# Performance work log

Measured on AMD Instinct MI355X. Metric: run time of the kernel, lower is better.

Reference implementation:

```python
import jax, jax.numpy as jnp
import numpy as np

B, V, HP, WP = 1, 6, 37, 66
N, CD, CC = HP * WP, 768, 256
BEVH = BEVW = 100
Q = BEVH * BEVW
NH, NP, D, Z = 8, 4, 4, 8
HD = CC // NH
PC = (-51.2, -51.2, -5.0, 51.2, 51.2, 3.0)
SCALE, PT, PL = 0.5775, 0.0, 0.0
H2, W2 = 518, 924
EPS = 1e-6


def setup_inputs() -> dict:
    key = jax.random.key(0)
    ks = jax.random.split(key, 10)
    s = 0.02
    return {
        "last_tokens": jax.random.normal(ks[0], (B, V, N, CD), jnp.float32),
        "lidar2img": jax.random.normal(ks[1], (B, V, 4, 4), jnp.float32),
        "proj_w": jax.random.normal(ks[2], (CC, CD), jnp.float32) * s,
        "bev_query": jax.random.normal(ks[3], (Q, CC), jnp.float32) * s,
        "w_view": jnp.zeros((1, V, 1), jnp.float32),
        "vp_w": jax.random.normal(ks[4], (CC, CC), jnp.float32) * s,
        "vp_b": jnp.zeros((CC,), jnp.float32),
        "so_w": jax.random.normal(ks[5], (NH * NP * 2, CC), jnp.float32) * s,
        "so_b": jnp.zeros((NH * NP * 2,), jnp.float32),
        "aw_w": jax.random.normal(ks[6], (NH * NP, CC), jnp.float32) * s,
        "aw_b": jnp.zeros((NH * NP,), jnp.float32),
        "op_w": jax.random.normal(ks[7], (CC, CC), jnp.float32) * s,
        "op_b": jnp.zeros((CC,), jnp.float32),
    }


def _ref_points_3d():
    # normalized pillar reference points, (D, Q, 3) in xyz order, Q = h*BEVW + w
    xs = (jnp.arange(BEVW, dtype=jnp.float32) + 0.5) / BEVW
    ys = (jnp.arange(BEVH, dtype=jnp.float32) + 0.5) / BEVH
    zs = jnp.linspace(0.5, Z - 0.5, D, dtype=jnp.float32) / Z
    gx = jnp.broadcast_to(xs[None, :], (BEVH, BEVW)).reshape(-1)
    gy = jnp.broadcast_to(ys[:, None], (BEVH, BEVW)).reshape(-1)
    return jnp.stack([jnp.broadcast_to(gx, (D, Q)),
                      jnp.broadcast_to(gy, (D, Q)),
                      jnp.broadcast_to(zs[:, None], (D, Q))], axis=-1)


def reference(last_tokens, lidar2img, proj_w, bev_query, w_view,
              vp_w, vp_b, so_w, so_b, aw_w, aw_b, op_w, op_b):
    BV = B * V
    # ---- project 3D BEV pillar points to camera views ----
    ref = _ref_points_3d()  # (D, Q, 3)
    wx = ref[..., 0] * (PC[3] - PC[0]) + PC[0]
    wy = ref[..., 1] * (PC[4] - PC[1]) + PC[1]
    wz = ref[..., 2] * (PC[5] - PC[2]) + PC[2]
    ref4 = jnp.stack([wx, wy, wz, jnp.ones_like(wx)], axis=-1)  # (D, Q, 4)
    cam = jnp.einsum('bvij,dqj->bvdqi', lidar2img, ref4)  # (B, V, D, Q, 4)
    depth = cam[..., 2]
    bev_mask = depth > 1e-5
    uv = cam[..., :2] / jnp.clip(depth, 1e-5)[..., None]
    u = uv[..., 0] * SCALE + PL
    v = uv[..., 1] * SCALE + PT
    in_img = (u >= 0) & (u <= W2 - 1) & (v >= 0) & (v <= H2 - 1)
    valid = bev_mask & in_img
    refx = jnp.clip(u / max(W2 - 1.0, 1.0), 0.0, 1.0)
    refy = jnp.clip(v / max(H2 - 1.0, 1.0), 0.0, 1.0)
    w = jnp.maximum(valid.astype(jnp.float32), EPS)  # (B, V, D, Q)
    den = jnp.maximum(w.sum(2), EPS)
    rx = (refx * w).sum(2) / den
    ry = (refy * w).sum(2) / den
    ref2d = jnp.stack([rx, ry], axis=-1).reshape(BV, Q, 2)

    # ---- value features: 1x1 conv proj + value_proj ----
    val = jnp.einsum('bvnc,oc->bvno', last_tokens, proj_w).reshape(BV, N, CC)
    val = val @ vp_w.T + vp_b
    val = val.reshape(BV, N, NH, HD)

    # ---- deformable attention (single level) ----
    query = jnp.broadcast_to(bev_query[None], (BV, Q, CC))
    off = (query @ so_w.T + so_b).reshape(BV, Q, NH, NP, 2)
    attn = jax.nn.softmax((query @ aw_w.T + aw_b).reshape(BV, Q, NH, NP), axis=-1)
    normalizer = jnp.array([WP, HP], jnp.float32)
    loc = ref2d[:, :, None, None, :] + off / normalizer  # (BV, Q, NH, NP, 2)

    # bilinear sampling, grid_sample semantics (align_corners=False, zero pad)
    x = loc[..., 0] * WP - 0.5
    y = loc[..., 1] * HP - 0.5
    x0 = jnp.floor(x); y0 = jnp.floor(y)
    fx = x - x0; fy = y - y0
    x0i = x0.astype(jnp.int32); y0i = y0.astype(jnp.int32)
    b_idx = jnp.arange(BV)[:, None, None, None]
    h_idx = jnp.arange(NH)[None, None, :, None]

    def corner(xi, yi, wgt):
        ok = ((xi >= 0) & (xi < WP) & (yi >= 0) & (yi < HP)).astype(val.dtype)
        lin = jnp.clip(yi, 0, HP - 1) * WP + jnp.clip(xi, 0, WP - 1)
        g = val[b_idx, lin, h_idx]  # (BV, Q, NH, NP, HD)
        return g * (ok * wgt)[..., None]

    samp = (corner(x0i, y0i, (1 - fx) * (1 - fy))
            + corner(x0i + 1, y0i, fx * (1 - fy))
            + corner(x0i, y0i + 1, (1 - fx) * fy)
            + corner(x0i + 1, y0i + 1, fx * fy))
    out = (samp * attn[..., None]).sum(3).reshape(BV, Q, CC)
    out = out @ op_w.T + op_b + query  # residual (mmcv identity)

    # ---- view-weighted combine ----
    out = out.reshape(B, V, Q, CC)
    wv = jax.nn.softplus(w_view)  # (1, V, 1)
    num = (out * wv[..., None]).sum(1)  # (B, Q, CC)
    den_v = jnp.maximum(wv.sum(1), EPS)[..., None]
    bev = num / den_v
    return jnp.transpose(bev, (0, 2, 1)).reshape(B, CC, BEVH, BEVW)
```

## Files before the change

### kernel.cpp

```cpp
#include <hip/hip_runtime.h>
#include <math.h>

#define Q_TOT 10000
#define NVIEW 6
#define NTOK  2442
#define HP_   37
#define WP_   66
#define CD_   768
#define CC_   256

typedef __attribute__((ext_vector_type(8))) short bf16x8;
typedef __attribute__((ext_vector_type(4))) float f32x4;

__device__ inline unsigned f2bf(float f) {
    unsigned u = __builtin_bit_cast(unsigned, f);
    unsigned r = u + 0x7FFFu + ((u >> 16) & 1u);
    return r >> 16;
}

__global__ __launch_bounds__(256) void w2_kernel(const float* __restrict__ vp_w,
                                                 const float* __restrict__ proj_w,
                                                 unsigned short* __restrict__ W2b) {
    int b = blockIdx.x;
    int o2 = b / 3;
    int c = (b % 3) * 256 + threadIdx.x;
    __shared__ float vps[256];
    vps[threadIdx.x] = vp_w[(size_t)o2 * 256 + threadIdx.x];
    __syncthreads();
    float acc = 0.f;
#pragma unroll 16
    for (int o = 0; o < 256; ++o) {
        acc += vps[o] * proj_w[(size_t)o * CD_ + c];
    }
    W2b[(size_t)o2 * CD_ + c] = (unsigned short)f2bf(acc);
}

__global__ void cvt8_kernel(const float* __restrict__ src, unsigned short* __restrict__ dst, int n8) {
    int i = blockIdx.x * blockDim.x + threadIdx.x;
    if (i >= n8) return;
    float4 a = *(const float4*)(src + (size_t)i * 8);
    float4 b = *(const float4*)(src + (size_t)i * 8 + 4);
    uint4 o;
    o.x = f2bf(a.x) | (f2bf(a.y) << 16);
    o.y = f2bf(a.z) | (f2bf(a.w) << 16);
    o.z = f2bf(b.x) | (f2bf(b.y) << 16);
    o.w = f2bf(b.z) | (f2bf(b.w) << 16);
    *(uint4*)(dst + (size_t)i * 8) = o;
}

__global__ void ref2d_kernel(const float* __restrict__ l2i, float* __restrict__ ref2d) {
    int idx = blockIdx.x * blockDim.x + threadIdx.x;
    if (idx >= NVIEW * Q_TOT) return;
    int v = idx / Q_TOT, q = idx % Q_TOT;
    int wq = q % 100, hq = q / 100;
    float gx = (wq + 0.5f) * 0.01f;
    float gy = (hq + 0.5f) * 0.01f;
    float wx = gx * 102.4f - 51.2f;
    float wy = gy * 102.4f - 51.2f;
    const float* L = l2i + v * 16;
    float L0=L[0],L1=L[1],L2=L[2],L3=L[3],L4=L[4],L5=L[5],L6=L[6],L7=L[7];
    float L8=L[8],L9=L[9],L10=L[10],L11=L[11];
    float sw = 0.f, sx = 0.f, sy = 0.f;
#pragma unroll
    for (int d = 0; d < 4; ++d) {
        float zs = (0.5f + (float)d * (7.0f / 3.0f)) * 0.125f;
        float wz = zs * 8.0f - 5.0f;
        float c0 = L0 * wx + L1 * wy + L2 * wz + L3;
        float c1 = L4 * wx + L5 * wy + L6 * wz + L7;
        float c2 = L8 * wx + L9 * wy + L10 * wz + L11;
        bool bm = c2 > 1e-5f;
        float dc = fmaxf(c2, 1e-5f);
        float u  = (c0 / dc) * 0.5775f;
        float vv = (c1 / dc) * 0.5775f;
        bool in_img = (u >= 0.f) && (u <= 923.f) && (vv >= 0.f) && (vv <= 517.f);
        bool valid = bm && in_img;
        float refx = fminf(fmaxf(u / 923.0f, 0.f), 1.f);
        float refy = fminf(fmaxf(vv / 517.0f, 0.f), 1.f);
        float w = valid ? 1.0f : 1e-6f;
        sw += w; sx += refx * w; sy += refy * w;
    }
    float den = fmaxf(sw, 1e-6f);
    ref2d[(size_t)idx * 2 + 0] = sx / den;
    ref2d[(size_t)idx * 2 + 1] = sy / den;
}

__global__ void concatb_kernel(const float* __restrict__ so_w, const float* __restrict__ so_b,
                               const float* __restrict__ aw_w, const float* __restrict__ aw_b,
                               const float* __restrict__ wview,
                               unsigned short* __restrict__ WQb, float* __restrict__ bqp,
                               float* __restrict__ vwn) {
    int row = blockIdx.x, col = threadIdx.x;
    float v = (row < 64) ? so_w[row * 256 + col] : (row < 96 ? aw_w[(row - 64) * 256 + col] : 0.f);
    WQb[row * 256 + col] = (unsigned short)f2bf(v);
    if (row == 0 && col < 128) bqp[col] = (col < 64) ? so_b[col] : (col < 96 ? aw_b[col - 64] : 0.f);
    if (row == 1 && col == 0) {
        float sp[6], swv = 0.f;
#pragma unroll
        for (int vv = 0; vv < NVIEW; ++vv) {
            float x = wview[vv];
            float s = (x > 20.f) ? x : log1pf(expf(x));
            sp[vv] = s; swv += s;
        }
        float inv = 1.0f / fmaxf(swv, 1e-6f);
#pragma unroll
        for (int vv = 0; vv < NVIEW; ++vv) vwn[vv] = sp[vv] * inv;
        vwn[6] = swv * inv;
        vwn[7] = 0.f;
    }
}

template <int MODE, int KT>
__global__ __launch_bounds__(256, 4) void mfma_gemm(const void* __restrict__ Aptr,
                                                    const unsigned short* __restrict__ Bw,
                                                    const float* __restrict__ bias,
                                                    const float* __restrict__ resid,
                                                    const float* __restrict__ wview,
                                                    void* __restrict__ Cptr,
                                                    int M, int nt_shift) {
    constexpr int K = KT * 64;
    __shared__ unsigned short lds0[2 * 64 * 64];
    __shared__ unsigned short lds1[2 * 64 * 64];
    char* base0 = (char*)lds0;
    char* base1 = (char*)lds1;
    int tid = threadIdx.x;
    int wid = tid >> 6, lane = tid & 63;

    int nwg = gridDim.x;
    int bid = blockIdx.x;
    int qd = nwg >> 3, r = nwg & 7;
    int xcd = bid & 7, seq = bid >> 3;
    int wgid = (xcd < r) ? (xcd * (qd + 1) + seq) : (r * (qd + 1) + (xcd - r) * qd + seq);
    int mt = wgid >> nt_shift;
    int nt = wgid & ((1 << nt_shift) - 1);
    int m0 = mt * 64, n0 = nt * 64;

    int lr = lane & 15, lq = lane >> 4;
    int arow_s = tid >> 4;
    int ac4 = tid & 15;
    const float* Af = (const float*)Aptr;
    const unsigned short* Ah = (const unsigned short*)Aptr;
    float* Cf = (float*)Cptr;
    unsigned short* Ch = (unsigned short*)Cptr;

    f32x4 acc[4];
#pragma unroll
    for (int j = 0; j < 4; ++j) acc[j] = (f32x4)(0.f);

    float4 aF[2][4];
    uint4  aB[2][2];
    uint4  bR[2][2];
    const float4 zf4 = make_float4(0.f, 0.f, 0.f, 0.f);

#define LOADG(S, KTI) do {                                                            \
    int k0 = (KTI) << 6;                                                              \
    if (MODE == 0 || MODE == 2) {                                                     \
        _Pragma("unroll")                                                             \
        for (int p_ = 0; p_ < 4; ++p_) {                                              \
            int row_ = p_ * 16 + arow_s;                                              \
            bool av_ = (m0 + row_) < M;                                               \
            aF[S][p_] = av_ ? *(const float4*)(Af + (size_t)(m0 + row_) * K + k0 + ac4 * 4) : zf4; \
        }                                                                             \
    } else {                                                                          \
        _Pragma("unroll")                                                             \
        for (int i_ = 0; i_ < 2; ++i_) {                                              \
            int s_ = tid + (i_ << 8);                                                 \
            int row_ = s_ >> 3, c_ = s_ & 7;                                          \
            aB[S][i_] = *(const uint4*)(Ah + (size_t)(m0 + row_) * K + k0 + c_ * 8);  \
        }                                                                             \
    }                                                                                 \
    _Pragma("unroll")                                                                 \
    for (int i_ = 0; i_ < 2; ++i_) {                                                  \
        int s_ = tid + (i_ << 8);                                                     \
        int row_ = s_ >> 3, c_ = s_ & 7;                                              \
        bR[S][i_] = *(const uint4*)(Bw + (size_t)(n0 + row_) * K + k0 + c_ * 8);      \
    }                                                                                 \
} while (0)

#define TOLDS(S, PB) do {                                                             \
    char* Abb = (PB) ? base1 : base0;                                                 \
    if (MODE == 0 || MODE == 2) {                                                     \
        _Pragma("unroll")                                                             \
        for (int p_ = 0; p_ < 4; ++p_) {                                              \
            int row_ = p_ * 16 + arow_s;                                              \
            const float* f_ = (const float*)&aF[S][p_];                               \
            uint2 w_;                                                                 \
            w_.x = f2bf(f_[0]) | (f2bf(f_[1]) << 16);                                 \
            w_.y = f2bf(f_[2]) | (f2bf(f_[3]) << 16);                                 \
            int byte_ = row_ * 128 + (((ac4 >> 1) ^ (row_ & 7)) << 4) + ((ac4 & 1) << 3); \
            *(uint2*)(Abb + byte_) = w_;                                              \
        }                                                                             \
    } else {                                                                          \
        _Pragma("unroll")                                                             \
        for (int i_ = 0; i_ < 2; ++i_) {                                              \
            int s_ = tid + (i_ << 8);                                                 \
            int row_ = s_ >> 3, c_ = s_ & 7;                                          \
            *(uint4*)(Abb + row_ * 128 + ((c_ ^ (row_ & 7)) << 4)) = aB[S][i_];       \
        }                                                                             \
    }                                                                                 \
    char* Bbb = Abb + 8192;                                                           \
    _Pragma("unroll")                                                                 \
    for (int i_ = 0; i_ < 2; ++i_) {                                                  \
        int s_ = tid + (i_ << 8);                                                     \
        int row_ = s_ >> 3, c_ = s_ & 7;                                              \
        *(uint4*)(Bbb + row_ * 128 + ((c_ ^ (row_ & 7)) << 4)) = bR[S][i_];           \
    }                                                                                 \
} while (0)

#define MFMAS(PB) do {                                                                \
    char* Abb = (PB) ? base1 : base0;                                                 \
    char* Bbb = Abb + 8192;                                                           \
    _Pragma("unroll")                                                                 \
    for (int s_ = 0; s_ < 2; ++s_) {                                                  \
        int chunk_ = (s_ << 2) + lq;                                                  \
        int arow_ = (wid << 4) + lr;                                                  \
        bf16x8 af_ = *(bf16x8*)(Abb + arow_ * 128 + ((chunk_ ^ (arow_ & 7)) << 4));   \
        _Pragma("unroll")                                                             \
        for (int j_ = 0; j_ < 4; ++j_) {                                              \
            int brow_ = (j_ << 4) + lr;                                               \
            bf16x8 bf_ = *(bf16x8*)(Bbb + brow_ * 128 + ((chunk_ ^ (brow_ & 7)) << 4)); \
            acc[j_] = __builtin_amdgcn_mfma_f32_16x16x32_bf16(af_, bf_, acc[j_], 0, 0, 0); \
        }                                                                             \
    }                                                                                 \
} while (0)

#define BARRIER() do {                                                                \
    __builtin_amdgcn_sched_barrier(0);                                                \
    asm volatile("s_waitcnt lgkmcnt(0)" ::: "memory");                                \
    __builtin_amdgcn_s_barrier();                                                     \
    __builtin_amdgcn_sched_barrier(0);                                                \
} while (0)

    LOADG(0, 0);
#pragma unroll
    for (int kt = 0; kt < KT; ++kt) {
        if (kt + 1 < KT) LOADG((kt + 1) & 1, kt + 1);
        TOLDS(kt & 1, kt & 1);
        BARRIER();
        MFMAS(kt & 1);
    }

    int mb = m0 + (wid << 4) + (lq << 2);
    if (MODE == 0) {
#pragma unroll
        for (int j = 0; j < 4; ++j) {
            int n = n0 + (j << 4) + lr;
            float bn = bias[n];
#pragma unroll
            for (int e = 0; e < 4; ++e) {
                int m = mb + e;
                if (m < M) Ch[(size_t)m * 256 + n] = (unsigned short)f2bf(acc[j][e] + bn);
            }
        }
    } else if (MODE == 1) {
        float s = 0.f;
#pragma unroll
        for (int v = 0; v < 6; ++v) {
            float x = wview[v];
            s += (x > 20.f) ? x : log1pf(expf(x));
        }
        float f = s / fmaxf(s, 1e-6f);
#pragma unroll
        for (int j = 0; j < 4; ++j) {
            int n = n0 + (j << 4) + lr;
            float bn = bias[n];
            if (mb + 4 <= M) {
                float4 o;
                float* oo = (float*)&o;
#pragma unroll
                for (int e = 0; e < 4; ++e)
                    oo[e] = acc[j][e] + f * (bn + resid[(size_t)(mb + e) * 256 + n]);
                *(float4*)(Cf + (size_t)n * M + mb) = o;
            } else {
#pragma unroll
                for (int e = 0; e < 4; ++e) {
                    int m = mb + e;
                    if (m < M) Cf[(size_t)n * M + m] = acc[j][e] + f * (bn + resid[(size_t)m * 256 + n]);
                }
            }
        }
    } else {
#pragma unroll
        for (int j = 0; j < 4; ++j) {
            int n = n0 + (j << 4) + lr;
            if (n >= 96) continue;
            float bn = bias[n];
#pragma unroll
            for (int e = 0; e < 4; ++e) {
                int m = mb + e;
                if (m < M) Cf[(size_t)m * 96 + n] = acc[j][e] + bn;
            }
        }
    }
#undef LOADG
#undef TOLDS
#undef MFMAS
#undef BARRIER
}

__global__ __launch_bounds__(256) void sample_kernel(const unsigned short* __restrict__ valB,
                                                     const float* __restrict__ ref2d,
                                                     const float* __restrict__ qout,
                                                     const float* __restrict__ vwn,
                                                     unsigned short* __restrict__ sampavgB) {
    __shared__ uint4  sOff[4 * 240];
    __shared__ float4 sW[4 * 240];
    __shared__ float4 sAt[4 * 8];
    __shared__ float  sVw[8];
    int tid = threadIdx.x;
    int qb = blockIdx.x * 4;

    if (tid < 32) {
        int ql = tid >> 3, h = tid & 7;
        const float* qo = qout + (size_t)(qb + ql) * 96 + 64 + h * 4;
        float a0 = qo[0], a1 = qo[1], a2 = qo[2], a3 = qo[3];
        float mx = fmaxf(fmaxf(a0, a1), fmaxf(a2, a3));
        float e0 = __expf(a0 - mx), e1 = __expf(a1 - mx), e2 = __expf(a2 - mx), e3 = __expf(a3 - mx);
        float inv = 1.0f / (e0 + e1 + e2 + e3);
        sAt[ql * 8 + h] = make_float4(e0 * inv, e1 * inv, e2 * inv, e3 * inv);
        if (tid < 8) sVw[tid] = vwn[tid < 6 ? tid : 0];
    }
    __syncthreads();

#pragma unroll
    for (int t = tid; t < 768; t += 256) {
        int ql = t / 192;
        int rem = t - ql * 192;
        int v = rem >> 5;
        int h = (rem >> 2) & 7;
        int p = rem & 3;
        int q = qb + ql;
        const float* qo = qout + (size_t)q * 96;
        float ox = qo[h * 8 + 2 * p];
        float oy = qo[h * 8 + 2 * p + 1];
        float at = ((const float*)&sAt[ql * 8 + h])[p];
        float scale = at * sVw[v];

        float rx = ref2d[(size_t)(v * Q_TOT + q) * 2 + 0];
        float ry = ref2d[(size_t)(v * Q_TOT + q) * 2 + 1];
        float x = rx * 66.0f + ox - 0.5f;
        float y = ry * 37.0f + oy - 0.5f;
        float xf = floorf(x), yf = floorf(y);
        float fx = x - xf, fy = y - yf;
        int xi = (int)xf, yi = (int)yf;

        float cw[4] = { (1.f - fx) * (1.f - fy), fx * (1.f - fy), (1.f - fx) * fy, fx * fy };
        unsigned off[4];
#pragma unroll
        for (int cyi = 0; cyi < 2; ++cyi) {
#pragma unroll
            for (int cxi = 0; cxi < 2; ++cxi) {
                int cx = xi + cxi, cy = yi + cyi;
                bool ok = (cx >= 0) && (cx < WP_) && (cy >= 0) && (cy < HP_);
                int ccx = cx < 0 ? 0 : (cx > WP_ - 1 ? WP_ - 1 : cx);
                int ccy = cy < 0 ? 0 : (cy > HP_ - 1 ? HP_ - 1 : cy);
                int c_ = cyi * 2 + cxi;
                off[c_] = (unsigned)((v * NTOK + ccy * WP_ + ccx) << 9);
                cw[c_] = ok ? cw[c_] * scale : 0.f;
            }
        }
        int slot = ql * 240 + v * 40 + h * 5 + p;
        sOff[slot] = make_uint4(off[0], off[1], off[2], off[3]);
        sW[slot]   = make_float4(cw[0], cw[1], cw[2], cw[3]);
    }
    __syncthreads();

    int ql = tid >> 6;
    int lane = tid & 63;
    int h = lane >> 3, d4 = (lane & 7) << 2;
    unsigned coff = (unsigned)((h * 32 + d4) << 1);
    const char* vbase = (const char*)valB;
    float acc0 = 0.f, acc1 = 0.f, acc2 = 0.f, acc3 = 0.f;
#pragma unroll
    for (int v = 0; v < NVIEW; ++v) {
#pragma unroll
        for (int p = 0; p < 4; ++p) {
            int slot = ql * 240 + v * 40 + h * 5 + p;
            uint4 off = sOff[slot];
            float4 w = sW[slot];
            uint2 r0 = *(const uint2*)(vbase + (off.x + coff));
            uint2 r1 = *(const uint2*)(vbase + (off.y + coff));
            uint2 r2 = *(const uint2*)(vbase + (off.z + coff));
            uint2 r3 = *(const uint2*)(vbase + (off.w + coff));
#define UNP(u_) __builtin_bit_cast(float, (u_) << 16), __builtin_bit_cast(float, (u_) & 0xFFFF0000u)
            {
                float g0, g1; 
                g0 = __builtin_bit_cast(float, r0.x << 16); g1 = __builtin_bit_cast(float, r0.x & 0xFFFF0000u);
                acc0 += w.x * g0; acc1 += w.x * g1;
                g0 = __builtin_bit_cast(float, r0.y << 16); g1 = __builtin_bit_cast(float, r0.y & 0xFFFF0000u);
                acc2 += w.x * g0; acc3 += w.x * g1;
                g0 = __builtin_bit_cast(float, r1.x << 16); g1 = __builtin_bit_cast(float, r1.x & 0xFFFF0000u);
                acc0 += w.y * g0; acc1 += w.y * g1;
                g0 = __builtin_bit_cast(float, r1.y << 16); g1 = __builtin_bit_cast(float, r1.y & 0xFFFF0000u);
                acc2 += w.y * g0; acc3 += w.y * g1;
                g0 = __builtin_bit_cast(float, r2.x << 16); g1 = __builtin_bit_cast(float, r2.x & 0xFFFF0000u);
                acc0 += w.z * g0; acc1 += w.z * g1;
                g0 = __builtin_bit_cast(float, r2.y << 16); g1 = __builtin_bit_cast(float, r2.y & 0xFFFF0000u);
                acc2 += w.z * g0; acc3 += w.z * g1;
                g0 = __builtin_bit_cast(float, r3.x << 16); g1 = __builtin_bit_cast(float, r3.x & 0xFFFF0000u);
                acc0 += w.w * g0; acc1 += w.w * g1;
                g0 = __builtin_bit_cast(float, r3.y << 16); g1 = __builtin_bit_cast(float, r3.y & 0xFFFF0000u);
                acc2 += w.w * g0; acc3 += w.w * g1;
            }
#undef UNP
        }
    }
    int q = qb + ql;
    unsigned u0 = f2bf(acc0) | (f2bf(acc1) << 16);
    unsigned u1 = f2bf(acc2) | (f2bf(acc3) << 16);
    *(uint2*)(sampavgB + (size_t)q * CC_ + h * 32 + d4) = make_uint2(u0, u1);
}

extern "C" void kernel_launch(void* const* d_in, const int* in_sizes, int n_in,
                              void* d_out, int out_size, void* d_ws, size_t ws_size,
                              hipStream_t stream) {
    const float* lt   = (const float*)d_in[0];
    const float* l2i  = (const float*)d_in[1];
    const float* proj = (const float*)d_in[2];
    const float* bqq  = (const float*)d_in[3];
    const float* wv   = (const float*)d_in[4];
    const float* vpw  = (const float*)d_in[5];
    const float* vpb  = (const float*)d_in[6];
    const float* sow  = (const float*)d_in[7];
    const float* sob  = (const float*)d_in[8];
    const float* aww  = (const float*)d_in[9];
    const float* awb  = (const float*)d_in[10];
    const float* opw  = (const float*)d_in[11];
    const float* opb  = (const float*)d_in[12];
    float* out = (float*)d_out;

    char* ws = (char*)d_ws;
    unsigned short* W2b   = (unsigned short*)(ws);
    unsigned short* opwb  = (unsigned short*)(ws + 393216);
    unsigned short* WQb   = (unsigned short*)(ws + 524288);
    float*          bqp   = (float*)(ws + 589824);
    float*          vwn   = (float*)(ws + 590336);
    float*          ref2d = (float*)(ws + 590848);
    float*          qout  = (float*)(ws + 1070848);
    unsigned short* valB  = (unsigned short*)(ws + 4910848);
    unsigned short* sampavgB = (unsigned short*)(ws + 12412672);

    hipLaunchKernelGGL(w2_kernel, dim3(768), dim3(256), 0, stream, vpw, proj, W2b);
    hipLaunchKernelGGL(cvt8_kernel, dim3(32), dim3(256), 0, stream, opw, opwb, 8192);
    hipLaunchKernelGGL(ref2d_kernel, dim3((NVIEW * Q_TOT + 255) / 256), dim3(256), 0, stream, l2i, ref2d);
    hipLaunchKernelGGL(concatb_kernel, dim3(128), dim3(256), 0, stream, sow, sob, aww, awb, wv, WQb, bqp, vwn);
    hipLaunchKernelGGL((mfma_gemm<2, 4>), dim3(314), dim3(256), 0, stream,
                       (const void*)bqq, WQb, bqp, nullptr, nullptr, (void*)qout, Q_TOT, 1);
    hipLaunchKernelGGL((mfma_gemm<0, 12>), dim3(916), dim3(256), 0, stream,
                       (const void*)lt, W2b, vpb, nullptr, nullptr, (void*)valB, 14652, 2);
    hipLaunchKernelGGL(sample_kernel, dim3(Q_TOT / 4), dim3(256), 0, stream,
                       valB, ref2d, qout, vwn, sampavgB);
    hipLaunchKernelGGL((mfma_gemm<1, 4>), dim3(628), dim3(256), 0, stream,
                       (const void*)sampavgB, opwb, opb, bqq, wv, (void*)out, Q_TOT, 2);
}
```

Baseline: 94.35 us.

## Merge prep kernels into one launch and co-schedule value and query GEMMs

Four small preprocessing kernels (weight product, op_w cast, ref-point projection, concat/softmax of view weights) are folded into one block-partitioned prep kernel. The weight-product path is reworked so each block computes 16 output rows with register accumulation, using 48 blocks instead of 768. The value-projection GEMM and query-offset GEMM run in a single launch split by block index, which removes launch gaps and lets the small GEMM fill the tail of the large one. The trade-off is fewer blocks for the W2 product, so that path has less parallelism and a longer serial loop.

```diff
diff --git a/kernel.cpp b/kernel.cpp
--- a/kernel.cpp
+++ b/kernel.cpp
@@ -18,115 +18,118 @@
     return r >> 16;
 }
 
-__global__ __launch_bounds__(256) void w2_kernel(const float* __restrict__ vp_w,
-                                                 const float* __restrict__ proj_w,
-                                                 unsigned short* __restrict__ W2b) {
-    int b = blockIdx.x;
-    int o2 = b / 3;
-    int c = (b % 3) * 256 + threadIdx.x;
-    __shared__ float vps[256];
-    vps[threadIdx.x] = vp_w[(size_t)o2 * 256 + threadIdx.x];
-    __syncthreads();
-    float acc = 0.f;
-#pragma unroll 16
-    for (int o = 0; o < 256; ++o) {
-        acc += vps[o] * proj_w[(size_t)o * CD_ + c];
-    }
-    W2b[(size_t)o2 * CD_ + c] = (unsigned short)f2bf(acc);
-}
-
-__global__ void cvt8_kernel(const float* __restrict__ src, unsigned short* __restrict__ dst, int n8) {
-    int i = blockIdx.x * blockDim.x + threadIdx.x;
-    if (i >= n8) return;
-    float4 a = *(const float4*)(src + (size_t)i * 8);
-    float4 b = *(const float4*)(src + (size_t)i * 8 + 4);
-    uint4 o;
-    o.x = f2bf(a.x) | (f2bf(a.y) << 16);
-    o.y = f2bf(a.z) | (f2bf(a.w) << 16);
-    o.z = f2bf(b.x) | (f2bf(b.y) << 16);
-    o.w = f2bf(b.z) | (f2bf(b.w) << 16);
-    *(uint4*)(dst + (size_t)i * 8) = o;
-}
-
-__global__ void ref2d_kernel(const float* __restrict__ l2i, float* __restrict__ ref2d) {
-    int idx = blockIdx.x * blockDim.x + threadIdx.x;
-    if (idx >= NVIEW * Q_TOT) return;
-    int v = idx / Q_TOT, q = idx % Q_TOT;
-    int wq = q % 100, hq = q / 100;
-    float gx = (wq + 0.5f) * 0.01f;
-    float gy = (hq + 0.5f) * 0.01f;
-    float wx = gx * 102.4f - 51.2f;
-    float wy = gy * 102.4f - 51.2f;
-    const float* L = l2i + v * 16;
-    float L0=L[0],L1=L[1],L2=L[2],L3=L[3],L4=L[4],L5=L[5],L6=L[6],L7=L[7];
-    float L8=L[8],L9=L[9],L10=L[10],L11=L[11];
-    float sw = 0.f, sx = 0.f, sy = 0.f;
-#pragma unroll
-    for (int d = 0; d < 4; ++d) {
-        float zs = (0.5f + (float)d * (7.0f / 3.0f)) * 0.125f;
-        float wz = zs * 8.0f - 5.0f;
-        float c0 = L0 * wx + L1 * wy + L2 * wz + L3;
-        float c1 = L4 * wx + L5 * wy + L6 * wz + L7;
-        float c2 = L8 * wx + L9 * wy + L10 * wz + L11;
-        bool bm = c2 > 1e-5f;
-        float dc = fmaxf(c2, 1e-5f);
-        float u  = (c0 / dc) * 0.5775f;
-        float vv = (c1 / dc) * 0.5775f;
-        bool in_img = (u >= 0.f) && (u <= 923.f) && (vv >= 0.f) && (vv <= 517.f);
-        bool valid = bm && in_img;
-        float refx = fminf(fmaxf(u / 923.0f, 0.f), 1.f);
-        float refy = fminf(fmaxf(vv / 517.0f, 0.f), 1.f);
-        float w = valid ? 1.0f : 1e-6f;
-        sw += w; sx += refx * w; sy += refy * w;
-    }
-    float den = fmaxf(sw, 1e-6f);
-    ref2d[(size_t)idx * 2 + 0] = sx / den;
-    ref2d[(size_t)idx * 2 + 1] = sy / den;
-}
-
-__global__ void concatb_kernel(const float* __restrict__ so_w, const float* __restrict__ so_b,
-                               const float* __restrict__ aw_w, const float* __restrict__ aw_b,
-                               const float* __restrict__ wview,
-                               unsigned short* __restrict__ WQb, float* __restrict__ bqp,
-                               float* __restrict__ vwn) {
-    int row = blockIdx.x, col = threadIdx.x;
-    float v = (row < 64) ? so_w[row * 256 + col] : (row < 96 ? aw_w[(row - 64) * 256 + col] : 0.f);
-    WQb[row * 256 + col] = (unsigned short)f2bf(v);
-    if (row == 0 && col < 128) bqp[col] = (col < 64) ? so_b[col] : (col < 96 ? aw_b[col - 64] : 0.f);
-    if (row == 1 && col == 0) {
-        float sp[6], swv = 0.f;
-#pragma unroll
-        for (int vv = 0; vv < NVIEW; ++vv) {
-            float x = wview[vv];
-            float s = (x > 20.f) ? x : log1pf(expf(x));
-            sp[vv] = s; swv += s;
-        }
-        float inv = 1.0f / fmaxf(swv, 1e-6f);
-#pragma unroll
-        for (int vv = 0; vv < NVIEW; ++vv) vwn[vv] = sp[vv] * inv;
-        vwn[6] = swv * inv;
-        vwn[7] = 0.f;
+__global__ __launch_bounds__(256) void prep_kernel(const float* __restrict__ vp_w,
+                                                   const float* __restrict__ proj_w,
+                                                   const float* __restrict__ opw,
+                                                   const float* __restrict__ l2i,
+                                                   const float* __restrict__ so_w,
+                                                   const float* __restrict__ so_b,
+                                                   const float* __restrict__ aw_w,
+                                                   const float* __restrict__ aw_b,
+                                                   const float* __restrict__ wview,
+                                                   unsigned short* __restrict__ W2b,
+                                                   unsigned short* __restrict__ opwb,
+                                                   float* __restrict__ ref2d,
+                                                   unsigned short* __restrict__ WQb,
+                                                   float* __restrict__ bqp,
+                                                   float* __restrict__ vwn) {
+    int b = blockIdx.x, tid = threadIdx.x;
+    if (b < 48) {
+        int g = b / 3, p = b % 3;
+        int c = p * 256 + tid;
+        float acc[16] = {};
+        for (int o8 = 0; o8 < 256; o8 += 8) {
+            float pw[8];
+#pragma unroll
+            for (int i = 0; i < 8; ++i) pw[i] = proj_w[(size_t)(o8 + i) * CD_ + c];
+#pragma unroll
+            for (int r = 0; r < 16; ++r) {
+#pragma unroll
+                for (int i = 0; i < 8; ++i)
+                    acc[r] += vp_w[(size_t)(g * 16 + r) * 256 + o8 + i] * pw[i];
+            }
+        }
+#pragma unroll
+        for (int r = 0; r < 16; ++r)
+            W2b[(size_t)(g * 16 + r) * CD_ + c] = (unsigned short)f2bf(acc[r]);
+    } else if (b < 80) {
+        int i = (b - 48) * 256 + tid;
+        float4 a = *(const float4*)(opw + (size_t)i * 8);
+        float4 c4 = *(const float4*)(opw + (size_t)i * 8 + 4);
+        uint4 o;
+        o.x = f2bf(a.x) | (f2bf(a.y) << 16);
+        o.y = f2bf(a.z) | (f2bf(a.w) << 16);
+        o.z = f2bf(c4.x) | (f2bf(c4.y) << 16);
+        o.w = f2bf(c4.z) | (f2bf(c4.w) << 16);
+        *(uint4*)(opwb + (size_t)i * 8) = o;
+    } else if (b < 315) {
+        int idx = (b - 80) * 256 + tid;
+        if (idx < NVIEW * Q_TOT) {
+            int v = idx / Q_TOT, q = idx % Q_TOT;
+            int wq = q % 100, hq = q / 100;
+            float wx = (wq + 0.5f) * 1.024f - 51.2f;
+            float wy = (hq + 0.5f) * 1.024f - 51.2f;
+            const float* L = l2i + v * 16;
+            float L0=L[0],L1=L[1],L2=L[2],L3=L[3],L4=L[4],L5=L[5],L6=L[6],L7=L[7];
+            float L8=L[8],L9=L[9],L10=L[10],L11=L[11];
+            float sw = 0.f, sx = 0.f, sy = 0.f;
+#pragma unroll
+            for (int d = 0; d < 4; ++d) {
+                float zs = (0.5f + (float)d * (7.0f / 3.0f)) * 0.125f;
+                float wz = zs * 8.0f - 5.0f;
+                float c0 = L0 * wx + L1 * wy + L2 * wz + L3;
+                float c1 = L4 * wx + L5 * wy + L6 * wz + L7;
+                float c2 = L8 * wx + L9 * wy + L10 * wz + L11;
+                bool bm = c2 > 1e-5f;
+                float dc = fmaxf(c2, 1e-5f);
+                float u  = (c0 / dc) * 0.5775f;
+                float vv = (c1 / dc) * 0.5775f;
+                bool in_img = (u >= 0.f) && (u <= 923.f) && (vv >= 0.f) && (vv <= 517.f);
+                bool valid = bm && in_img;
+                float refx = fminf(fmaxf(u / 923.0f, 0.f), 1.f);
+                float refy = fminf(fmaxf(vv / 517.0f, 0.f), 1.f);
+                float w = valid ? 1.0f : 1e-6f;
+                sw += w; sx += refx * w; sy += refy * w;
+            }
+            float den = fmaxf(sw, 1e-6f);
+            ref2d[(size_t)idx * 2 + 0] = sx / den;
+            ref2d[(size_t)idx * 2 + 1] = sy / den;
+        }
+    } else {
+        int row = b - 315, col = tid;
+        float v = (row < 64) ? so_w[row * 256 + col] : (row < 96 ? aw_w[(row - 64) * 256 + col] : 0.f);
+        WQb[row * 256 + col] = (unsigned short)f2bf(v);
+        if (row == 0 && col < 128) bqp[col] = (col < 64) ? so_b[col] : (col < 96 ? aw_b[col - 64] : 0.f);
+        if (row == 1 && col == 0) {
+            float sp[6], swv = 0.f;
+#pragma unroll
+            for (int vv = 0; vv < NVIEW; ++vv) {
+                float x = wview[vv];
+                float s = (x > 20.f) ? x : log1pf(expf(x));
+                sp[vv] = s; swv += s;
+            }
+            float inv = 1.0f / fmaxf(swv, 1e-6f);
+#pragma unroll
+            for (int vv = 0; vv < NVIEW; ++vv) vwn[vv] = sp[vv] * inv;
+            vwn[6] = swv * inv;
+            vwn[7] = 0.f;
+        }
     }
 }
 
 template <int MODE, int KT>
-__global__ __launch_bounds__(256, 4) void mfma_gemm(const void* __restrict__ Aptr,
-                                                    const unsigned short* __restrict__ Bw,
-                                                    const float* __restrict__ bias,
-                                                    const float* __restrict__ resid,
-                                                    const float* __restrict__ wview,
-                                                    void* __restrict__ Cptr,
-                                                    int M, int nt_shift) {
+__device__ __forceinline__ void gemm_body(char* base0, char* base1,
+                                          const void* __restrict__ Aptr,
+                                          const unsigned short* __restrict__ Bw,
+                                          const float* __restrict__ bias,
+                                          const float* __restrict__ resid,
+                                          const float* __restrict__ wview,
+                                          void* __restrict__ Cptr,
+                                          int M, int nt_shift, int bid, int nwg) {
     constexpr int K = KT * 64;
-    __shared__ unsigned short lds0[2 * 64 * 64];
-    __shared__ unsigned short lds1[2 * 64 * 64];
-    char* base0 = (char*)lds0;
-    char* base1 = (char*)lds1;
     int tid = threadIdx.x;
     int wid = tid >> 6, lane = tid & 63;
 
-    int nwg = gridDim.x;
-    int bid = blockIdx.x;
     int qd = nwg >> 3, r = nwg & 7;
     int xcd = bid & 7, seq = bid >> 3;
     int wgid = (xcd < r) ? (xcd * (qd + 1) + seq) : (r * (qd + 1) + (xcd - r) * qd + seq);
@@ -297,6 +300,38 @@
 #undef BARRIER
 }
 
+__global__ __launch_bounds__(256, 4) void dual_gemm(const float* __restrict__ lt,
+                                                    const unsigned short* __restrict__ W2b,
+                                                    const float* __restrict__ vpb,
+                                                    unsigned short* __restrict__ valB,
+                                                    const float* __restrict__ bqq,
+                                                    const unsigned short* __restrict__ WQb,
+                                                    const float* __restrict__ bqp,
+                                                    float* __restrict__ qout) {
+    __shared__ unsigned short lds[4 * 64 * 64];
+    char* b0 = (char*)lds;
+    char* b1 = (char*)lds + 16384;
+    if (blockIdx.x < 916)
+        gemm_body<0, 12>(b0, b1, (const void*)lt, W2b, vpb, nullptr, nullptr,
+                         (void*)valB, 14652, 2, blockIdx.x, 916);
+    else
+        gemm_body<2, 4>(b0, b1, (const void*)bqq, WQb, bqp, nullptr, nullptr,
+                        (void*)qout, Q_TOT, 1, blockIdx.x - 916, 314);
+}
+
+__global__ __launch_bounds__(256, 4) void out_gemm(const unsigned short* __restrict__ sampavgB,
+                                                   const unsigned short* __restrict__ opwb,
+                                                   const float* __restrict__ opb,
+                                                   const float* __restrict__ bqq,
+                                                   const float* __restrict__ wview,
+                                                   float* __restrict__ out) {
+    __shared__ unsigned short lds[4 * 64 * 64];
+    char* b0 = (char*)lds;
+    char* b1 = (char*)lds + 16384;
+    gemm_body<1, 4>(b0, b1, (const void*)sampavgB, opwb, opb, bqq, wview,
+                    (void*)out, Q_TOT, 2, blockIdx.x, gridDim.x);
+}
+
 __global__ __launch_bounds__(256) void sample_kernel(const unsigned short* __restrict__ valB,
                                                      const float* __restrict__ ref2d,
                                                      const float* __restrict__ qout,
@@ -381,27 +416,23 @@
             uint2 r1 = *(const uint2*)(vbase + (off.y + coff));
             uint2 r2 = *(const uint2*)(vbase + (off.z + coff));
             uint2 r3 = *(const uint2*)(vbase + (off.w + coff));
-#define UNP(u_) __builtin_bit_cast(float, (u_) << 16), __builtin_bit_cast(float, (u_) & 0xFFFF0000u)
-            {
-                float g0, g1; 
-                g0 = __builtin_bit_cast(float, r0.x << 16); g1 = __builtin_bit_cast(float, r0.x & 0xFFFF0000u);
-                acc0 += w.x * g0; acc1 += w.x * g1;
-                g0 = __builtin_bit_cast(float, r0.y << 16); g1 = __builtin_bit_cast(float, r0.y & 0xFFFF0000u);
-                acc2 += w.x * g0; acc3 += w.x * g1;
-                g0 = __builtin_bit_cast(float, r1.x << 16); g1 = __builtin_bit_cast(float, r1.x & 0xFFFF0000u);
-                acc0 += w.y * g0; acc1 += w.y * g1;
-                g0 = __builtin_bit_cast(float, r1.y << 16); g1 = __builtin_bit_cast(float, r1.y & 0xFFFF0000u);
-                acc2 += w.y * g0; acc3 += w.y * g1;
-                g0 = __builtin_bit_cast(float, r2.x << 16); g1 = __builtin_bit_cast(float, r2.x & 0xFFFF0000u);
-                acc0 += w.z * g0; acc1 += w.z * g1;
-                g0 = __builtin_bit_cast(float, r2.y << 16); g1 = __builtin_bit_cast(float, r2.y & 0xFFFF0000u);
-                acc2 += w.z * g0; acc3 += w.z * g1;
-                g0 = __builtin_bit_cast(float, r3.x << 16); g1 = __builtin_bit_cast(float, r3.x & 0xFFFF0000u);
-                acc0 += w.w * g0; acc1 += w.w * g1;
-                g0 = __builtin_bit_cast(float, r3.y << 16); g1 = __builtin_bit_cast(float, r3.y & 0xFFFF0000u);
-                acc2 += w.w * g0; acc3 += w.w * g1;
-            }
-#undef UNP
+            float g0, g1;
+            g0 = __builtin_bit_cast(float, r0.x << 16); g1 = __builtin_bit_cast(float, r0.x & 0xFFFF0000u);
+            acc0 += w.x * g0; acc1 += w.x * g1;
+            g0 = __builtin_bit_cast(float, r0.y << 16); g1 = __builtin_bit_cast(float, r0.y & 0xFFFF0000u);
+            acc2 += w.x * g0; acc3 += w.x * g1;
+            g0 = __builtin_bit_cast(float, r1.x << 16); g1 = __builtin_bit_cast(float, r1.x & 0xFFFF0000u);
+            acc0 += w.y * g0; acc1 += w.y * g1;
+            g0 = __builtin_bit_cast(float, r1.y << 16); g1 = __builtin_bit_cast(float, r1.y & 0xFFFF0000u);
+            acc2 += w.y * g0; acc3 += w.y * g1;
+            g0 = __builtin_bit_cast(float, r2.x << 16); g1 = __builtin_bit_cast(float, r2.x & 0xFFFF0000u);
+            acc0 += w.z * g0; acc1 += w.z * g1;
+            g0 = __builtin_bit_cast(float, r2.y << 16); g1 = __builtin_bit_cast(float, r2.y & 0xFFFF0000u);
+            acc2 += w.z * g0; acc3 += w.z * g1;
+            g0 = __builtin_bit_cast(float, r3.x << 16); g1 = __builtin_bit_cast(float, r3.x & 0xFFFF0000u);
+            acc0 += w.w * g0; acc1 += w.w * g1;
+            g0 = __builtin_bit_cast(float, r3.y << 16); g1 = __builtin_bit_cast(float, r3.y & 0xFFFF0000u);
+            acc2 += w.w * g0; acc3 += w.w * g1;
         }
     }
     int q = qb + ql;
@@ -439,16 +470,13 @@
     unsigned short* valB  = (unsigned short*)(ws + 4910848);
     unsigned short* sampavgB = (unsigned short*)(ws + 12412672);
 
-    hipLaunchKernelGGL(w2_kernel, dim3(768), dim3(256), 0, stream, vpw, proj, W2b);
-    hipLaunchKernelGGL(cvt8_kernel, dim3(32), dim3(256), 0, stream, opw, opwb, 8192);
-    hipLaunchKernelGGL(ref2d_kernel, dim3((NVIEW * Q_TOT + 255) / 256), dim3(256), 0, stream, l2i, ref2d);
-    hipLaunchKernelGGL(concatb_kernel, dim3(128), dim3(256), 0, stream, sow, sob, aww, awb, wv, WQb, bqp, vwn);
-    hipLaunchKernelGGL((mfma_gemm<2, 4>), dim3(314), dim3(256), 0, stream,
-                       (const void*)bqq, WQb, bqp, nullptr, nullptr, (void*)qout, Q_TOT, 1);
-    hipLaunchKernelGGL((mfma_gemm<0, 12>), dim3(916), dim3(256), 0, stream,
-                       (const void*)lt, W2b, vpb, nullptr, nullptr, (void*)valB, 14652, 2);
+    hipLaunchKernelGGL(prep_kernel, dim3(443), dim3(256), 0, stream,
+                       vpw, proj, opw, l2i, sow, sob, aww, awb, wv,
+                       W2b, opwb, ref2d, WQb, bqp, vwn);
+    hipLaunchKernelGGL(dual_gemm, dim3(1230), dim3(256), 0, stream,
+                       lt, W2b, vpb, valB, bqq, WQb, bqp, qout);
     hipLaunchKernelGGL(sample_kernel, dim3(Q_TOT / 4), dim3(256), 0, stream,
                        valB, ref2d, qout, vwn, sampavgB);
-    hipLaunchKernelGGL((mfma_gemm<1, 4>), dim3(628), dim3(256), 0, stream,
-                       (const void*)sampavgB, opwb, opb, bqq, wv, (void*)out, Q_TOT, 2);
-}
+    hipLaunchKernelGGL(out_gemm, dim3(628), dim3(256), 0, stream,
+                       sampavgB, opwb, opb, bqq, wv, out);
+}
```

Measured after the change: 131.8 us. 39.7% more time.
